# Kernel tuning notes

Hardware: AMD Instinct MI355X
Metric: run time of the kernel (lower is better)

Reference implementation:

```python
import jax, jax.numpy as jnp
import numpy as np
import math

B, C, N = 4, 128, 4096
GROUPS = 8
EPS = 1e-5


def setup_inputs() -> dict:
    key = jax.random.key(0)
    ks = jax.random.split(key, 7)
    x = jax.random.normal(ks[0], (B, C, N), dtype=jnp.float32)
    gn_w = jnp.ones((C,), dtype=jnp.float32)
    gn_b = jnp.zeros((C,), dtype=jnp.float32)
    # Conv1d with kernel_size=1 is a per-position linear map: weight [out, in]
    s_qkv = 1.0 / math.sqrt(C)
    w_qkv = jax.random.uniform(ks[1], (3 * C, C), jnp.float32, -s_qkv, s_qkv)
    b_qkv = jax.random.uniform(ks[2], (3 * C,), jnp.float32, -s_qkv, s_qkv)
    w_out = jax.random.uniform(ks[3], (C, C), jnp.float32, -s_qkv, s_qkv)
    b_out = jax.random.uniform(ks[4], (C,), jnp.float32, -s_qkv, s_qkv)
    return {"x": x, "gn_w": gn_w, "gn_b": gn_b, "w_qkv": w_qkv,
            "b_qkv": b_qkv, "w_out": w_out, "b_out": b_out}


def reference(x, gn_w, gn_b, w_qkv, b_qkv, w_out, b_out):
    b, c, n = x.shape
    # GroupNorm(8, c): normalize over (channels-in-group, n)
    xg = x.reshape(b, GROUPS, c // GROUPS, n)
    mean = jnp.mean(xg, axis=(2, 3), keepdims=True)
    var = jnp.var(xg, axis=(2, 3), keepdims=True)
    h = ((xg - mean) * jax.lax.rsqrt(var + EPS)).reshape(b, c, n)
    h = h * gn_w[None, :, None] + gn_b[None, :, None]
    # 1x1 conv QKV projection
    qkv = jnp.einsum('oc,bcn->bon', w_qkv, h) + b_qkv[None, :, None]
    q, k, v = jnp.split(qkv, 3, axis=1)  # each [b, c, n]
    scale = 1.0 / math.sqrt(c)
    attn = jax.nn.softmax(jnp.einsum('bci,bcj->bij', q, k) * scale, axis=-1)
    # h[b,c,i] = sum_j v[b,c,j] * attn[b,i,j]  (torch: bmm(v, attn^T))
    h2 = jnp.einsum('bcj,bij->bci', v, attn)
    out = jnp.einsum('oc,bcn->bon', w_out, h2) + b_out[None, :, None]
    return out + x
```

## Files before the change

### kernel.cpp

```cpp
#include <hip/hip_runtime.h>
#include <hip/hip_bf16.h>


#define CH 128
#define SEQ 4096
#define EPSV 1e-5f
#define QSCALE (0.08838834764831845f * 1.4426950408889634f)
#define SMAX 24.0f

typedef unsigned short u16;
typedef unsigned int u32;
typedef __attribute__((ext_vector_type(8))) short short8;
typedef __attribute__((ext_vector_type(4))) u32 u32x4;
typedef __attribute__((ext_vector_type(4))) float floatx4;
typedef __attribute__((ext_vector_type(16))) float floatx16;

__device__ __forceinline__ float bf2f(u16 h) {
    return __uint_as_float(((u32)h) << 16);
}
__device__ __forceinline__ float lo16(u32 wd) { return __uint_as_float(wd << 16); }
__device__ __forceinline__ float hi16(u32 wd) { return __uint_as_float(wd & 0xffff0000u); }
__device__ __forceinline__ u16 f2bf(float f) {
    u32 u = __float_as_uint(f);
    return (u16)((u + 0x7fffu + ((u >> 16) & 1u)) >> 16);
}
__device__ __forceinline__ u32 pkbf(float a, float b) {
    __hip_bfloat162 h = __float22bfloat162_rn(make_float2(a, b));
    u32 r;
    __builtin_memcpy(&r, &h, 4);
    return r;
}
__device__ __forceinline__ floatx4 mfma16(short8 a, short8 b, floatx4 c) {
    return __builtin_amdgcn_mfma_f32_16x16x32_bf16(a, b, c, 0, 0, 0);
}
__device__ __forceinline__ floatx16 mfma32(short8 a, short8 b, floatx16 c) {
    return __builtin_amdgcn_mfma_f32_32x32x16_bf16(a, b, c, 0, 0, 0);
}
__device__ __forceinline__ void pl32(u32& a, u32& b) {
    asm("v_permlane32_swap_b32 %0, %1" : "+v"(a), "+v"(b));
}
__device__ __forceinline__ short8 mk8(u32 a, u32 b, u32 c, u32 d) {
    u32x4 v = (u32x4){a, b, c, d};
    return __builtin_bit_cast(short8, v);
}

__global__ void gn_wconv(const float* __restrict__ x, float* __restrict__ part,
                         const float* __restrict__ w_qkv, const float* __restrict__ w_out,
                         u16* __restrict__ wq, u16* __restrict__ wo) {
    if (blockIdx.x >= 256) {
        int i = (blockIdx.x - 256) * 256 + threadIdx.x;
        if (i < 49152) wq[i] = f2bf(w_qkv[i]);
        else           wo[i - 49152] = f2bf(w_out[i - 49152]);
        return;
    }
    int bg = blockIdx.x >> 3, sub = blockIdx.x & 7;
    const float4* xp = (const float4*)(x + (size_t)bg * 65536 + sub * 8192);
    float s = 0.f, sq = 0.f;
    for (int r = 0; r < 8; ++r) {
        float4 v = xp[threadIdx.x + 256 * r];
        s  += v.x + v.y + v.z + v.w;
        sq += v.x*v.x + v.y*v.y + v.z*v.z + v.w*v.w;
    }
    for (int off = 32; off; off >>= 1) {
        s  += __shfl_down(s, off, 64);
        sq += __shfl_down(sq, off, 64);
    }
    __shared__ float ls[8];
    int wave = threadIdx.x >> 6, lane = threadIdx.x & 63;
    if (lane == 0) { ls[wave*2] = s; ls[wave*2+1] = sq; }
    __syncthreads();
    if (threadIdx.x == 0) {
        float ts = 0.f, tq = 0.f;
        for (int w = 0; w < 4; ++w) { ts += ls[w*2]; tq += ls[w*2+1]; }
        part[blockIdx.x * 2]     = ts;
        part[blockIdx.x * 2 + 1] = tq;
    }
}

__global__ __launch_bounds__(256, 2) void qkv_fused(
        const float* __restrict__ x, const float* __restrict__ gw,
        const float* __restrict__ gb, const float* __restrict__ part,
        const u16* __restrict__ wq, const float* __restrict__ b_qkv,
        u16* __restrict__ qT, u16* __restrict__ kT, u16* __restrict__ v) {
    __shared__ __align__(16) u16 hT[32 * 136];
    __shared__ __align__(16) u16 qbuf[32 * 132];
    __shared__ __align__(16) u16 kbuf[32 * 132];
    __shared__ __align__(16) u16 vbuf[128 * 36];
    __shared__ float cw[128], cb[128];
    int bx = blockIdx.x;
    int nc = bx & 127, b = bx >> 7;
    int n0 = nc * 32;
    int t = threadIdx.x, w = t >> 6, lane = t & 63;
    int quad = lane >> 4, l15 = lane & 15;

    if (t < 128) {
        int g = t >> 4;
        float s = 0.f, sq = 0.f;
        #pragma unroll
        for (int u = 0; u < 8; ++u) {
            s  += part[((b * 8 + g) * 8 + u) * 2];
            sq += part[((b * 8 + g) * 8 + u) * 2 + 1];
        }
        float mean = s / 65536.f;
        float rstd = rsqrtf(sq / 65536.f - mean * mean + EPSV);
        float wgt = gw[t] * rstd;
        cw[t] = wgt;
        cb[t] = gb[t] - mean * wgt;
    }

    short8 wf[6][4];
    float bqk[6];
    #pragma unroll
    for (int j = 0; j < 6; ++j) {
        int orow = (w * 6 + j) * 16 + l15;
        #pragma unroll
        for (int kt = 0; kt < 4; ++kt)
            wf[j][kt] = *(const short8*)(wq + orow * 128 + kt * 32 + quad * 8);
        bqk[j] = b_qkv[orow];
    }
    __syncthreads();

    #pragma unroll
    for (int r = 0; r < 4; ++r) {
        int u = r * 256 + t;
        int c = u >> 3, col = (u & 7) * 4;
        float wgt = cw[c], bs = cb[c];
        float4 xv = *(const float4*)(x + ((size_t)(b * 128 + c)) * SEQ + n0 + col);
        hT[(col + 0) * 136 + c] = f2bf(fmaf(xv.x, wgt, bs));
        hT[(col + 1) * 136 + c] = f2bf(fmaf(xv.y, wgt, bs));
        hT[(col + 2) * 136 + c] = f2bf(fmaf(xv.z, wgt, bs));
        hT[(col + 3) * 136 + c] = f2bf(fmaf(xv.w, wgt, bs));
    }
    __syncthreads();

    #pragma unroll
    for (int nt = 0; nt < 2; ++nt) {
        short8 hf[4];
        #pragma unroll
        for (int kt = 0; kt < 4; ++kt)
            hf[kt] = *(const short8*)(hT + (nt * 16 + l15) * 136 + kt * 32 + quad * 8);
        floatx4 acc[6];
        #pragma unroll
        for (int j = 0; j < 6; ++j) acc[j] = (floatx4)0.f;
        #pragma unroll
        for (int kt = 0; kt < 4; ++kt)
            #pragma unroll
            for (int j = 0; j < 6; ++j) {
                if (w * 6 + j < 16) acc[j] = mfma16(hf[kt], wf[j][kt], acc[j]);
                else                acc[j] = mfma16(wf[j][kt], hf[kt], acc[j]);
            }
        #pragma unroll
        for (int j = 0; j < 6; ++j) {
            int T = w * 6 + j;
            if (T < 8) {
                int o = T * 16 + l15;
                #pragma unroll
                for (int r = 0; r < 4; ++r)
                    qbuf[(nt * 16 + quad * 4 + r) * 132 + o] =
                        f2bf((acc[j][r] + bqk[j]) * QSCALE);
            } else if (T < 16) {
                int o = (T - 8) * 16 + l15;
                #pragma unroll
                for (int r = 0; r < 4; ++r)
                    kbuf[(nt * 16 + quad * 4 + r) * 132 + o] =
                        f2bf(acc[j][r] + bqk[j]);
            } else {
                #pragma unroll
                for (int r = 0; r < 4; ++r) {
                    int ov = (T - 16) * 16 + quad * 4 + r;
                    vbuf[ov * 36 + nt * 16 + l15] = f2bf(acc[j][r] + b_qkv[256 + ov]);
                }
            }
        }
    }
    __syncthreads();

    {
        u16* qg = qT + ((size_t)b * SEQ + n0) * CH;
        u16* kg = kT + ((size_t)b * SEQ + n0) * CH;
        #pragma unroll
        for (int rep = 0; rep < 2; ++rep) {
            int idx = rep * 256 + t;
            int n = idx >> 4, c8 = (idx & 15) * 8;
            *(uint4*)(qg + n * CH + c8) = *(const uint4*)(qbuf + n * 132 + c8);
            *(uint4*)(kg + n * CH + c8) = *(const uint4*)(kbuf + n * 132 + c8);
        }
        #pragma unroll
        for (int rep = 0; rep < 2; ++rep) {
            int idx = rep * 256 + t;
            int c = idx >> 2, n8 = (idx & 3) * 8;
            *(uint4*)(v + ((size_t)(b * CH + c)) * SEQ + n0 + n8) =
                *(const uint4*)(vbuf + c * 36 + n8);
        }
    }
}

__global__ __launch_bounds__(512, 2) void flash_attn(
        const u16* __restrict__ qT, const u16* __restrict__ kT,
        const u16* __restrict__ v, u16* __restrict__ partO,
        float* __restrict__ lbuf) {
    __shared__ __align__(16) char smem[71680];
    u16* qts = (u16*)smem;
    u16* lds2 = (u16*)smem;

    int bx = blockIdx.x;
    int js = bx & 7, iblk = (bx >> 3) & 15, b = bx >> 7;
    int t = threadIdx.x, w = t >> 6, lane = t & 63;
    int il = lane & 31, h = lane >> 5;
    int i0 = iblk * 256, j0 = js * 512;

    int tj = t >> 4, tc8 = (t & 15) * 8;
    int tv = t >> 3, vc8 = (t & 7) * 8;

    {
        const u16* qb = qT + ((size_t)b * SEQ + i0) * CH;
        for (int r = 0; r < 8; ++r) {
            int u = r * 512 + t;
            int i = u >> 4, c16 = u & 15;
            *(uint4*)(qts + i * 136 + c16 * 8) =
                *(const uint4*)(qb + (size_t)i * CH + c16 * 8);
        }
    }
    __syncthreads();
    short8 qf[8];
    #pragma unroll
    for (int kc = 0; kc < 8; ++kc)
        qf[kc] = *(const short8*)(qts + (w * 32 + il) * 136 + kc * 16 + h * 8);
    __syncthreads();

    const u16* kTb = kT + ((size_t)b * SEQ + j0) * CH;
    const u16* vb  = v  + (size_t)b * CH * SEQ + j0;

    {
        u16* kts0 = (u16*)smem;
        u16* vts0 = kts0 + 8704;
        #pragma unroll
        for (int r = 0; r < 2; ++r)
            *(uint4*)(kts0 + (r * 32 + tj) * 136 + tc8) =
                *(const uint4*)(kTb + (size_t)(r * 32 + tj) * CH + tc8);
        #pragma unroll
        for (int r = 0; r < 2; ++r)
            *(uint4*)(vts0 + (r * 64 + tv) * 72 + vc8) =
                *(const uint4*)(vb + (size_t)(r * 64 + tv) * SEQ + vc8);
    }
    __syncthreads();

    float l_part = 0.f;
    floatx16 o[4];
    #pragma unroll
    for (int ct = 0; ct < 4; ++ct) o[ct] = (floatx16)0.f;

    for (int ch = 0; ch < 8; ++ch) {
        u16* kts = (u16*)(smem + (ch & 1) * 35840);
        u16* vts = kts + 8704;
        u16* ktsN = (u16*)(smem + ((ch + 1) & 1) * 35840);
        u16* vtsN = ktsN + 8704;
        int jb1 = (ch + 1) * 64;
        bool pf = (ch < 7);

        uint4 kreg[2];
        if (pf) {
            #pragma unroll
            for (int r = 0; r < 2; ++r)
                kreg[r] = *(const uint4*)(kTb + (size_t)(jb1 + r * 32 + tj) * CH + tc8);
        }

        short8 pfr[4];
        #pragma unroll
        for (int jt = 0; jt < 2; ++jt) {
            floatx16 s = (floatx16)(-SMAX);
            #pragma unroll
            for (int kc = 0; kc < 8; ++kc) {
                short8 kf = *(const short8*)(kts + (jt * 32 + il) * 136 + kc * 16 + h * 8);
                s = mfma32(kf, qf[kc], s);
            }
            float p[16];
            #pragma unroll
            for (int r = 0; r < 16; ++r) p[r] = __builtin_amdgcn_exp2f(s[r]);
            l_part += ((((p[0]+p[1])+(p[2]+p[3])) + ((p[4]+p[5])+(p[6]+p[7])))
                    +  (((p[8]+p[9])+(p[10]+p[11])) + ((p[12]+p[13])+(p[14]+p[15]))));
            u32 a0 = pkbf(p[0],  p[1]),  a1 = pkbf(p[2],  p[3]);
            u32 a2 = pkbf(p[4],  p[5]),  a3 = pkbf(p[6],  p[7]);
            u32 b0 = pkbf(p[8],  p[9]),  b1 = pkbf(p[10], p[11]);
            u32 b2 = pkbf(p[12], p[13]), b3 = pkbf(p[14], p[15]);
            pl32(a0, a2); pl32(a1, a3);
            pl32(b0, b2); pl32(b1, b3);
            pfr[2 * jt]     = mk8(a0, a1, a2, a3);
            pfr[2 * jt + 1] = mk8(b0, b1, b2, b3);
        }

        uint4 vreg[2];
        if (pf) {
            #pragma unroll
            for (int r = 0; r < 2; ++r)
                vreg[r] = *(const uint4*)(vb + (size_t)(r * 64 + tv) * SEQ + jb1 + vc8);
        }

        __builtin_amdgcn_s_setprio(1);
        #pragma unroll
        for (int ct = 0; ct < 4; ++ct) {
            const u16* vrow = vts + (ct * 32 + il) * 72;
            short8 vf0 = *(const short8*)(vrow + h * 8);
            short8 vf1 = *(const short8*)(vrow + 16 + h * 8);
            short8 vf2 = *(const short8*)(vrow + 32 + h * 8);
            short8 vf3 = *(const short8*)(vrow + 48 + h * 8);
            o[ct] = mfma32(vf0, pfr[0], o[ct]);
            o[ct] = mfma32(vf1, pfr[1], o[ct]);
            o[ct] = mfma32(vf2, pfr[2], o[ct]);
            o[ct] = mfma32(vf3, pfr[3], o[ct]);
        }
        __builtin_amdgcn_s_setprio(0);

        if (pf) {
            #pragma unroll
            for (int r = 0; r < 2; ++r)
                *(uint4*)(ktsN + (r * 32 + tj) * 136 + tc8) = kreg[r];
            #pragma unroll
            for (int r = 0; r < 2; ++r)
                *(uint4*)(vtsN + (r * 64 + tv) * 72 + vc8) = vreg[r];
        }
        __syncthreads();
    }

    #pragma unroll
    for (int ct = 0; ct < 4; ++ct)
        #pragma unroll
        for (int g = 0; g < 4; ++g) {
            uint2 pk2 = make_uint2(pkbf(o[ct][4*g+0], o[ct][4*g+1]),
                                   pkbf(o[ct][4*g+2], o[ct][4*g+3]));
            *(uint2*)(lds2 + (w * 32 + il) * 132 + ct * 32 + 8 * g + 4 * h) = pk2;
        }
    __syncthreads();
    u16* pb = partO + (((size_t)(js * 4 + b)) * 4096 + i0) * 128;
    #pragma unroll
    for (int rep = 0; rep < 8; ++rep) {
        int idx = rep * 512 + t;
        int i = idx >> 4, c8 = (idx & 15) * 8;
        *(uint4*)(pb + i * 128 + c8) = *(const uint4*)(lds2 + i * 132 + c8);
    }
    l_part += __shfl_xor(l_part, 32, 64);
    if (lane < 32)
        lbuf[((size_t)(js * 4 + b)) * 4096 + i0 + w * 32 + il] = l_part;
}

__global__ __launch_bounds__(256, 2) void merge_out(
        const u16* __restrict__ partO, const float* __restrict__ lbuf,
        const u16* __restrict__ wo, const float* __restrict__ b_out,
        const float* __restrict__ x, float* __restrict__ out) {
    __shared__ __align__(16) u16 h2T[32 * 136];
    __shared__ float fac[32];
    int bx = blockIdx.x;
    int qtr = bx & 3, iblk = (bx >> 2) & 31, b = bx >> 7;
    int gi0 = iblk * 128 + qtr * 32;
    int t = threadIdx.x, w = t >> 6, lane = t & 63;
    int quad = lane >> 4, l15 = lane & 15;

    short8 wf[2][4];
    #pragma unroll
    for (int j = 0; j < 2; ++j)
        #pragma unroll
        for (int kt = 0; kt < 4; ++kt)
            wf[j][kt] = *(const short8*)(wo + ((w * 2 + j) * 16 + l15) * 128 + kt * 32 + quad * 8);

    if (t < 32) {
        int gi = gi0 + t;
        float lv = 0.f;
        #pragma unroll
        for (int s = 0; s < 8; ++s)
            lv += lbuf[((size_t)(s * 4 + b)) * 4096 + gi];
        fac[t] = 1.f / lv;
    }
    __syncthreads();

    {
        int il = t >> 3, oct = t & 7;
        int gi = gi0 + il;
        float accv[16];
        #pragma unroll
        for (int e = 0; e < 16; ++e) accv[e] = 0.f;
        for (int s = 0; s < 8; ++s) {
            const u16* pb = partO + (((size_t)(s * 4 + b)) * 4096 + gi) * 128
                            + oct * 16;
            uint4 lo = *(const uint4*)(pb);
            uint4 hi = *(const uint4*)(pb + 8);
            accv[0]  += lo16(lo.x); accv[1]  += hi16(lo.x);
            accv[2]  += lo16(lo.y); accv[3]  += hi16(lo.y);
            accv[4]  += lo16(lo.z); accv[5]  += hi16(lo.z);
            accv[6]  += lo16(lo.w); accv[7]  += hi16(lo.w);
            accv[8]  += lo16(hi.x); accv[9]  += hi16(hi.x);
            accv[10] += lo16(hi.y); accv[11] += hi16(hi.y);
            accv[12] += lo16(hi.z); accv[13] += hi16(hi.z);
            accv[14] += lo16(hi.w); accv[15] += hi16(hi.w);
        }
        float fs = fac[il];
        #pragma unroll
        for (int e = 0; e < 16; ++e) accv[e] *= fs;
        uint4 lo = make_uint4(pkbf(accv[0],  accv[1]),  pkbf(accv[2],  accv[3]),
                              pkbf(accv[4],  accv[5]),  pkbf(accv[6],  accv[7]));
        uint4 hi = make_uint4(pkbf(accv[8],  accv[9]),  pkbf(accv[10], accv[11]),
                              pkbf(accv[12], accv[13]), pkbf(accv[14], accv[15]));
        *(uint4*)(h2T + il * 136 + oct * 16)     = lo;
        *(uint4*)(h2T + il * 136 + oct * 16 + 8) = hi;
    }
    __syncthreads();

    floatx4 acc[2][2];
    #pragma unroll
    for (int j = 0; j < 2; ++j) { acc[j][0] = (floatx4)0.f; acc[j][1] = (floatx4)0.f; }
    #pragma unroll
    for (int nt = 0; nt < 2; ++nt)
        #pragma unroll
        for (int kt = 0; kt < 4; ++kt) {
            short8 hf = *(const short8*)(h2T + (nt * 16 + l15) * 136 + kt * 32 + quad * 8);
            acc[0][nt] = mfma16(wf[0][kt], hf, acc[0][nt]);
            acc[1][nt] = mfma16(wf[1][kt], hf, acc[1][nt]);
        }

    int n_base = gi0;
    #pragma unroll
    for (int j = 0; j < 2; ++j)
        #pragma unroll
        for (int r = 0; r < 4; ++r) {
            int o = w * 32 + j * 16 + quad * 4 + r;
            float bo = b_out[o];
            #pragma unroll
            for (int nt = 0; nt < 2; ++nt) {
                int n = n_base + nt * 16 + l15;
                size_t idx = ((size_t)(b * 128 + o)) * SEQ + n;
                out[idx] = acc[j][nt][r] + bo + x[idx];
            }
        }
}

extern "C" void kernel_launch(void* const* d_in, const int* in_sizes, int n_in,
                              void* d_out, int out_size, void* d_ws, size_t ws_size,
                              hipStream_t stream) {
    const float* x     = (const float*)d_in[0];
    const float* gn_w  = (const float*)d_in[1];
    const float* gn_b  = (const float*)d_in[2];
    const float* w_qkv = (const float*)d_in[3];
    const float* b_qkv = (const float*)d_in[4];
    const float* w_out = (const float*)d_in[5];
    const float* b_out = (const float*)d_in[6];
    float* out = (float*)d_out;

    char* ws = (char*)d_ws;
    float* part = (float*)ws;
    u16*  wq  = (u16*)(ws + 4096);
    u16*  wo  = (u16*)(ws + 102400);
    u16*  qT  = (u16*)(ws + 135168);
    u16*  kT  = (u16*)(ws + 4329472);
    u16*  v   = (u16*)(ws + 8523776);
    u16*  pO  = (u16*)(ws + 12718080);
    float* lb = (float*)(ws + 46272512);

    gn_wconv<<<512, 256, 0, stream>>>(x, part, w_qkv, w_out, wq, wo);
    qkv_fused<<<512, 256, 0, stream>>>(x, gn_w, gn_b, part, wq, b_qkv, qT, kT, v);
    flash_attn<<<512, 512, 0, stream>>>(qT, kT, v, pO, lb);
    merge_out<<<512, 256, 0, stream>>>(pO, lb, wo, b_out, x, out);
}
```

Before: 79.65 us.

## Load K tiles directly to LDS with XOR swizzle, shrink attention blocks

```diff
diff --git a/kernel.cpp b/kernel.cpp
--- a/kernel.cpp
+++ b/kernel.cpp
@@ -42,6 +42,11 @@
 __device__ __forceinline__ short8 mk8(u32 a, u32 b, u32 c, u32 d) {
     u32x4 v = (u32x4){a, b, c, d};
     return __builtin_bit_cast(short8, v);
+}
+__device__ __forceinline__ void gl_lds16(const u16* g, u16* l) {
+    __builtin_amdgcn_global_load_lds(
+        (const __attribute__((address_space(1))) u32*)g,
+        (__attribute__((address_space(3))) u32*)l, 16, 0, 0);
 }
 
 __global__ void gn_wconv(const float* __restrict__ x, float* __restrict__ part,
@@ -195,27 +200,30 @@
     }
 }
 
-__global__ __launch_bounds__(512, 2) void flash_attn(
+__global__ __launch_bounds__(256, 3) void flash_attn(
         const u16* __restrict__ qT, const u16* __restrict__ kT,
         const u16* __restrict__ v, u16* __restrict__ partO,
         float* __restrict__ lbuf) {
-    __shared__ __align__(16) char smem[71680];
+    __shared__ __align__(16) char smem[49152];
     u16* qts = (u16*)smem;
     u16* lds2 = (u16*)smem;
+    u16* vts = (u16*)(smem + 32768);
 
     int bx = blockIdx.x;
-    int js = bx & 7, iblk = (bx >> 3) & 15, b = bx >> 7;
+    int js = bx & 7, iblk = (bx >> 3) & 31, b = bx >> 8;
     int t = threadIdx.x, w = t >> 6, lane = t & 63;
     int il = lane & 31, h = lane >> 5;
-    int i0 = iblk * 256, j0 = js * 512;
-
-    int tj = t >> 4, tc8 = (t & 15) * 8;
-    int tv = t >> 3, vc8 = (t & 7) * 8;
+    int i0 = iblk * 128, j0 = js * 512;
+    int sw8 = il & 7;
+
+    int lrow = lane >> 4, kslot = lane & 15;
+    int vc = t >> 3, vslot = t & 7;
+    int vswr = vslot ^ (vc & 7);
 
     {
         const u16* qb = qT + ((size_t)b * SEQ + i0) * CH;
         for (int r = 0; r < 8; ++r) {
-            int u = r * 512 + t;
+            int u = r * 256 + t;
             int i = u >> 4, c16 = u & 15;
             *(uint4*)(qts + i * 136 + c16 * 8) =
                 *(const uint4*)(qb + (size_t)i * CH + c16 * 8);
@@ -232,16 +240,19 @@
     const u16* vb  = v  + (size_t)b * CH * SEQ + j0;
 
     {
-        u16* kts0 = (u16*)smem;
-        u16* vts0 = kts0 + 8704;
-        #pragma unroll
-        for (int r = 0; r < 2; ++r)
-            *(uint4*)(kts0 + (r * 32 + tj) * 136 + tc8) =
-                *(const uint4*)(kTb + (size_t)(r * 32 + tj) * CH + tc8);
-        #pragma unroll
-        for (int r = 0; r < 2; ++r)
-            *(uint4*)(vts0 + (r * 64 + tv) * 72 + vc8) =
-                *(const uint4*)(vb + (size_t)(r * 64 + tv) * SEQ + vc8);
+        u16* kb = (u16*)smem + (w * 16) * 128;
+        #pragma unroll
+        for (int r = 0; r < 4; ++r) {
+            int row = w * 16 + r * 4 + lrow;
+            int sg = kslot ^ (row & 7);
+            gl_lds16(kTb + (size_t)row * CH + sg * 8, kb + r * 4 * 128);
+        }
+        #pragma unroll
+        for (int r = 0; r < 4; ++r) {
+            int c = r * 32 + vc;
+            uint4 vv = *(const uint4*)(vb + (size_t)c * SEQ + vslot * 8);
+            *(uint4*)(vts + c * 64 + vswr * 8) = vv;
+        }
     }
     __syncthreads();
 
@@ -251,18 +262,18 @@
     for (int ct = 0; ct < 4; ++ct) o[ct] = (floatx16)0.f;
 
     for (int ch = 0; ch < 8; ++ch) {
-        u16* kts = (u16*)(smem + (ch & 1) * 35840);
-        u16* vts = kts + 8704;
-        u16* ktsN = (u16*)(smem + ((ch + 1) & 1) * 35840);
-        u16* vtsN = ktsN + 8704;
+        const u16* kts = (const u16*)(smem + (ch & 1) * 16384);
+        bool pf = (ch < 7);
         int jb1 = (ch + 1) * 64;
-        bool pf = (ch < 7);
-
-        uint4 kreg[2];
+
         if (pf) {
-            #pragma unroll
-            for (int r = 0; r < 2; ++r)
-                kreg[r] = *(const uint4*)(kTb + (size_t)(jb1 + r * 32 + tj) * CH + tc8);
+            u16* kb = (u16*)(smem + ((ch + 1) & 1) * 16384) + (w * 16) * 128;
+            #pragma unroll
+            for (int r = 0; r < 4; ++r) {
+                int row = w * 16 + r * 4 + lrow;
+                int sg = kslot ^ (row & 7);
+                gl_lds16(kTb + (size_t)(jb1 + row) * CH + sg * 8, kb + r * 4 * 128);
+            }
         }
 
         short8 pfr[4];
@@ -271,7 +282,8 @@
             floatx16 s = (floatx16)(-SMAX);
             #pragma unroll
             for (int kc = 0; kc < 8; ++kc) {
-                short8 kf = *(const short8*)(kts + (jt * 32 + il) * 136 + kc * 16 + h * 8);
+                short8 kf = *(const short8*)(kts + (jt * 32 + il) * 128
+                                             + ((kc * 2 + h) ^ sw8) * 8);
                 s = mfma32(kf, qf[kc], s);
             }
             float p[16];
@@ -289,21 +301,22 @@
             pfr[2 * jt + 1] = mk8(b0, b1, b2, b3);
         }
 
-        uint4 vreg[2];
+        uint4 vreg[4];
         if (pf) {
             #pragma unroll
-            for (int r = 0; r < 2; ++r)
-                vreg[r] = *(const uint4*)(vb + (size_t)(r * 64 + tv) * SEQ + jb1 + vc8);
+            for (int r = 0; r < 4; ++r)
+                vreg[r] = *(const uint4*)(vb + (size_t)(r * 32 + vc) * SEQ
+                                          + jb1 + vslot * 8);
         }
 
         __builtin_amdgcn_s_setprio(1);
         #pragma unroll
         for (int ct = 0; ct < 4; ++ct) {
-            const u16* vrow = vts + (ct * 32 + il) * 72;
-            short8 vf0 = *(const short8*)(vrow + h * 8);
-            short8 vf1 = *(const short8*)(vrow + 16 + h * 8);
-            short8 vf2 = *(const short8*)(vrow + 32 + h * 8);
-            short8 vf3 = *(const short8*)(vrow + 48 + h * 8);
+            const u16* vrow = vts + (ct * 32 + il) * 64;
+            short8 vf0 = *(const short8*)(vrow + ((0 + h) ^ sw8) * 8);
+            short8 vf1 = *(const short8*)(vrow + ((2 + h) ^ sw8) * 8);
+            short8 vf2 = *(const short8*)(vrow + ((4 + h) ^ sw8) * 8);
+            short8 vf3 = *(const short8*)(vrow + ((6 + h) ^ sw8) * 8);
             o[ct] = mfma32(vf0, pfr[0], o[ct]);
             o[ct] = mfma32(vf1, pfr[1], o[ct]);
             o[ct] = mfma32(vf2, pfr[2], o[ct]);
@@ -311,15 +324,13 @@
         }
         __builtin_amdgcn_s_setprio(0);
 
+        __syncthreads();
         if (pf) {
             #pragma unroll
-            for (int r = 0; r < 2; ++r)
-                *(uint4*)(ktsN + (r * 32 + tj) * 136 + tc8) = kreg[r];
-            #pragma unroll
-            for (int r = 0; r < 2; ++r)
-                *(uint4*)(vtsN + (r * 64 + tv) * 72 + vc8) = vreg[r];
-        }
-        __syncthreads();
+            for (int r = 0; r < 4; ++r)
+                *(uint4*)(vts + (r * 32 + vc) * 64 + vswr * 8) = vreg[r];
+            __syncthreads();
+        }
     }
 
     #pragma unroll
@@ -334,7 +345,7 @@
     u16* pb = partO + (((size_t)(js * 4 + b)) * 4096 + i0) * 128;
     #pragma unroll
     for (int rep = 0; rep < 8; ++rep) {
-        int idx = rep * 512 + t;
+        int idx = rep * 256 + t;
         int i = idx >> 4, c8 = (idx & 15) * 8;
         *(uint4*)(pb + i * 128 + c8) = *(const uint4*)(lds2 + i * 132 + c8);
     }
@@ -456,6 +467,6 @@
 
     gn_wconv<<<512, 256, 0, stream>>>(x, part, w_qkv, w_out, wq, wo);
     qkv_fused<<<512, 256, 0, stream>>>(x, gn_w, gn_b, part, wq, b_qkv, qT, kT, v);
-    flash_attn<<<512, 512, 0, stream>>>(qT, kT, v, pO, lb);
+    flash_attn<<<1024, 256, 0, stream>>>(qT, kT, v, pO, lb);
     merge_out<<<512, 256, 0, stream>>>(pO, lb, wo, b_out, x, out);
 }
```

Measured after the change: 128.3 us. +61.1%, slower.
